# Optimization experiments

Measured on AMD Instinct MI355X. Metric: run time of the kernel, lower is better.

Reference implementation:

```python
import jax, jax.numpy as jnp
import numpy as np

HIDDEN_DIM = 128
NEIGHBOR_K = 2
N_ROWS = 1_000_000
BATCH = 262_144


def setup_inputs() -> dict:
    key = jax.random.key(0)
    k1, k2, k3, k4 = jax.random.split(key, 4)
    D = HIDDEN_DIM
    cat = D * (2 * NEIGHBOR_K + 1)  # 640
    x_rows = jax.random.normal(k1, (N_ROWS, D), dtype=jnp.float32)
    seed_indices = jax.random.randint(k2, (BATCH,), 0, N_ROWS)
    # torch.nn.Linear params: W [out, in], b [out]
    W1 = jax.random.normal(k3, (D, cat), dtype=jnp.float32) * (1.0 / np.sqrt(cat))
    b1 = jnp.zeros((D,), dtype=jnp.float32)
    W2 = jax.random.normal(k4, (D, D), dtype=jnp.float32) * (1.0 / np.sqrt(D))
    b2 = jnp.zeros((D,), dtype=jnp.float32)
    return {"x_rows": x_rows, "seed_indices": seed_indices,
            "W1": W1, "b1": b1, "W2": W2, "b2": b2}


def reference(x_rows, seed_indices, W1, b1, W2, b2):
    N, D = x_rows.shape
    B = seed_indices.shape[0]
    offsets = jnp.arange(-NEIGHBOR_K, NEIGHBOR_K + 1)  # [2k+1]
    idx = jnp.clip(seed_indices[:, None] + offsets[None, :], 0, N - 1)  # [B, 2k+1]
    # gather neighbor rows and flatten -> same as torch.cat(chunks, dim=-1)
    x_cat = x_rows[idx].reshape(B, (2 * NEIGHBOR_K + 1) * D)  # [B, 5D]
    h = jax.nn.relu(x_cat @ W1.T + b1)  # [B, D]
    return h @ W2.T + b2  # [B, D]
```

## Files before the change

kernel.cpp:

```cpp
#include <hip/hip_runtime.h>
#include <hip/hip_bf16.h>

#define D 128
#define CAT 640
#define BM 32
#define KS1 20
#define KS2 4
#define W1F_ELEMS 81920
#define W2F_ELEMS 16384

typedef __attribute__((ext_vector_type(8))) short bf16x8;
typedef __attribute__((ext_vector_type(4))) short short4v;
typedef __attribute__((ext_vector_type(4))) float f32x4;

static __device__ __forceinline__ unsigned short f32_to_bf16(float f) {
    unsigned u = __float_as_uint(f);
    unsigned r = u + 0x7FFFu + ((u >> 16) & 1u);
    return (unsigned short)(r >> 16);
}

__global__ void prep_frags(const float* __restrict__ W1, const float* __restrict__ W2,
                           unsigned short* __restrict__ W1f, unsigned short* __restrict__ W2f) {
    int f = blockIdx.x * 256 + threadIdx.x;
    if (f < W1F_ELEMS) {
        int e = f & 7, l = (f >> 3) & 63, j16 = (f >> 9) & 7, ks = f >> 12;
        int o = j16 * 16 + (l & 15);
        int k = ks * 32 + ((l >> 4) << 3) + e;
        W1f[f] = f32_to_bf16(W1[o * CAT + k]);
    } else if (f < W1F_ELEMS + W2F_ELEMS) {
        int f2 = f - W1F_ELEMS;
        int e = f2 & 7, l = (f2 >> 3) & 63, j16 = (f2 >> 9) & 7, ks = f2 >> 12;
        int o = j16 * 16 + (l & 15);
        int k = ks * 32 + ((l >> 4) << 3) + e;
        W2f[f2] = f32_to_bf16(W2[o * D + k]);
    }
}

__global__ __launch_bounds__(256) void rowmlp_kernel(
    const float* __restrict__ x_rows, const int* __restrict__ seeds,
    const unsigned short* __restrict__ W1f, const float* __restrict__ b1,
    const unsigned short* __restrict__ W2f, const float* __restrict__ b2,
    float* __restrict__ out, int B, int Nrows)
{
    __shared__ __align__(16) unsigned short Abuf[BM * CAT];
    __shared__ __align__(16) unsigned short Hbuf[BM * D];
    __shared__ int sseed[BM];

    const int tid = threadIdx.x;
    const int blk = blockIdx.x;

    if (tid < BM) sseed[tid] = seeds[blk * BM + tid];
    __syncthreads();

    {
        const int lane32 = tid & 31;
        const int segbase = tid >> 5;
        #pragma unroll
        for (int it = 0; it < BM * 5 / 8; ++it) {
            int seg = it * 8 + segbase;
            int row = seg / 5;
            int j = seg - row * 5;
            int idx = sseed[row] + j - 2;
            idx = idx < 0 ? 0 : (idx >= Nrows ? Nrows - 1 : idx);
            float4 v = *((const float4*)(x_rows + (size_t)idx * D) + lane32);
            short4v p;
            p.x = (short)f32_to_bf16(v.x);
            p.y = (short)f32_to_bf16(v.y);
            p.z = (short)f32_to_bf16(v.z);
            p.w = (short)f32_to_bf16(v.w);
            int kshort = j * D + lane32 * 4;
            int off = row * CAT + (kshort ^ ((row & 7) << 3));
            *(short4v*)(&Abuf[off]) = p;
        }
    }
    __syncthreads();

    const int wave = tid >> 6;
    const int l    = tid & 63;
    const int l15  = l & 15;
    const int lhi  = l >> 4;

    f32x4 acc[2][2] = {};
    #pragma unroll
    for (int ks = 0; ks < KS1; ++ks) {
        bf16x8 a[2], b[2];
        #pragma unroll
        for (int m = 0; m < 2; ++m) {
            int row = m * 16 + l15;
            int kshort = ks * 32 + lhi * 8;
            a[m] = *(const bf16x8*)(&Abuf[row * CAT + (kshort ^ ((row & 7) << 3))]);
        }
        #pragma unroll
        for (int n = 0; n < 2; ++n) {
            int j16 = wave * 2 + n;
            b[n] = ((const bf16x8*)W1f)[(ks * 8 + j16) * 64 + l];
        }
        #pragma unroll
        for (int m = 0; m < 2; ++m)
            #pragma unroll
            for (int n = 0; n < 2; ++n)
                acc[m][n] = __builtin_amdgcn_mfma_f32_16x16x32_bf16(a[m], b[n], acc[m][n], 0, 0, 0);
    }

    #pragma unroll
    for (int n = 0; n < 2; ++n) {
        int col = wave * 32 + n * 16 + l15;
        float bias = b1[col];
        #pragma unroll
        for (int m = 0; m < 2; ++m) {
            #pragma unroll
            for (int r = 0; r < 4; ++r) {
                float v = acc[m][n][r] + bias;
                v = v > 0.f ? v : 0.f;
                int row = m * 16 + lhi * 4 + r;
                Hbuf[row * D + (col ^ ((row & 7) << 3))] = f32_to_bf16(v);
            }
        }
    }
    __syncthreads();

    f32x4 acc2[2][2] = {};
    #pragma unroll
    for (int ks = 0; ks < KS2; ++ks) {
        bf16x8 a[2], b[2];
        #pragma unroll
        for (int m = 0; m < 2; ++m) {
            int row = m * 16 + l15;
            int kshort = ks * 32 + lhi * 8;
            a[m] = *(const bf16x8*)(&Hbuf[row * D + (kshort ^ ((row & 7) << 3))]);
        }
        #pragma unroll
        for (int n = 0; n < 2; ++n) {
            int j16 = wave * 2 + n;
            b[n] = ((const bf16x8*)W2f)[(ks * 8 + j16) * 64 + l];
        }
        #pragma unroll
        for (int m = 0; m < 2; ++m)
            #pragma unroll
            for (int n = 0; n < 2; ++n)
                acc2[m][n] = __builtin_amdgcn_mfma_f32_16x16x32_bf16(a[m], b[n], acc2[m][n], 0, 0, 0);
    }

    #pragma unroll
    for (int n = 0; n < 2; ++n) {
        int col = wave * 32 + n * 16 + l15;
        float bias = b2[col];
        #pragma unroll
        for (int m = 0; m < 2; ++m) {
            #pragma unroll
            for (int r = 0; r < 4; ++r) {
                int row = m * 16 + lhi * 4 + r;
                out[(size_t)(blk * BM + row) * D + col] = acc2[m][n][r] + bias;
            }
        }
    }
}

extern "C" void kernel_launch(void* const* d_in, const int* in_sizes, int n_in,
                              void* d_out, int out_size, void* d_ws, size_t ws_size,
                              hipStream_t stream) {
    const float* x_rows = (const float*)d_in[0];
    const int*   seeds  = (const int*)d_in[1];
    const float* W1     = (const float*)d_in[2];
    const float* b1     = (const float*)d_in[3];
    const float* W2     = (const float*)d_in[4];
    const float* b2     = (const float*)d_in[5];
    float* out = (float*)d_out;

    int Nrows = in_sizes[0] / D;
    int B = in_sizes[1];

    unsigned short* W1f = (unsigned short*)d_ws;
    unsigned short* W2f = W1f + W1F_ELEMS;

    prep_frags<<<(W1F_ELEMS + W2F_ELEMS + 255) / 256, 256, 0, stream>>>(W1, W2, W1f, W2f);
    rowmlp_kernel<<<B / BM, 256, 0, stream>>>(x_rows, seeds, W1f, b1, W2f, b2, out, B, Nrows);
}
```

Measured before the change: 197.2 us.

## Load gathered rows straight into MFMA A fragments, one 16-row tile per wave

Removes the shared-memory staging buffer for the gathered input. Each wave now owns 16 batch rows and loads its MFMA A operands directly from global memory, converting to bf16 in registers, and computes all 128 output columns itself. This eliminates the LDS write/read round trip and one block barrier, and shrinks shared memory so more blocks can be resident. In exchange, each wave reads all of W1/W2 for every 16 rows, so weight-fragment traffic per row doubles. The direct global loads are 32-byte chunks per lane rather than fully coalesced 512-byte rows.

```diff
diff --git a/kernel.cpp b/kernel.cpp
--- a/kernel.cpp
+++ b/kernel.cpp
@@ -3,14 +3,12 @@
 
 #define D 128
 #define CAT 640
-#define BM 32
 #define KS1 20
 #define KS2 4
 #define W1F_ELEMS 81920
 #define W2F_ELEMS 16384
 
 typedef __attribute__((ext_vector_type(8))) short bf16x8;
-typedef __attribute__((ext_vector_type(4))) short short4v;
 typedef __attribute__((ext_vector_type(4))) float f32x4;
 
 static __device__ __forceinline__ unsigned short f32_to_bf16(float f) {
@@ -40,118 +38,84 @@
     const float* __restrict__ x_rows, const int* __restrict__ seeds,
     const unsigned short* __restrict__ W1f, const float* __restrict__ b1,
     const unsigned short* __restrict__ W2f, const float* __restrict__ b2,
-    float* __restrict__ out, int B, int Nrows)
+    float* __restrict__ out, int Nrows)
 {
-    __shared__ __align__(16) unsigned short Abuf[BM * CAT];
-    __shared__ __align__(16) unsigned short Hbuf[BM * D];
-    __shared__ int sseed[BM];
+    __shared__ __align__(16) unsigned short Hbuf[4][16 * D];
 
     const int tid = threadIdx.x;
     const int blk = blockIdx.x;
+    const int g   = tid >> 6;
+    const int l   = tid & 63;
+    const int l15 = l & 15;
+    const int lhi = l >> 4;
 
-    if (tid < BM) sseed[tid] = seeds[blk * BM + tid];
-    __syncthreads();
+    const int sd = seeds[blk * 64 + g * 16 + l15];
+    unsigned roff[5];
+    #pragma unroll
+    for (int j = 0; j < 5; ++j) {
+        int idx = sd + j - 2;
+        idx = idx < 0 ? 0 : (idx >= Nrows ? Nrows - 1 : idx);
+        roff[j] = (unsigned)idx * (D * 4);
+    }
+    const char* xb = (const char*)x_rows;
+    const bf16x8* W1v = (const bf16x8*)W1f;
+    const bf16x8* W2v = (const bf16x8*)W2f;
 
-    {
-        const int lane32 = tid & 31;
-        const int segbase = tid >> 5;
+    f32x4 acc[8] = {};
+    #pragma unroll
+    for (int ks = 0; ks < KS1; ++ks) {
+        const int j = ks >> 2;
+        const float4* p = (const float4*)(xb + roff[j] + (ks & 3) * 128 + lhi * 32);
+        float4 p0 = p[0];
+        float4 p1 = p[1];
+        bf16x8 a;
+        a[0] = (short)f32_to_bf16(p0.x); a[1] = (short)f32_to_bf16(p0.y);
+        a[2] = (short)f32_to_bf16(p0.z); a[3] = (short)f32_to_bf16(p0.w);
+        a[4] = (short)f32_to_bf16(p1.x); a[5] = (short)f32_to_bf16(p1.y);
+        a[6] = (short)f32_to_bf16(p1.z); a[7] = (short)f32_to_bf16(p1.w);
         #pragma unroll
-        for (int it = 0; it < BM * 5 / 8; ++it) {
-            int seg = it * 8 + segbase;
-            int row = seg / 5;
-            int j = seg - row * 5;
-            int idx = sseed[row] + j - 2;
-            idx = idx < 0 ? 0 : (idx >= Nrows ? Nrows - 1 : idx);
-            float4 v = *((const float4*)(x_rows + (size_t)idx * D) + lane32);
-            short4v p;
-            p.x = (short)f32_to_bf16(v.x);
-            p.y = (short)f32_to_bf16(v.y);
-            p.z = (short)f32_to_bf16(v.z);
-            p.w = (short)f32_to_bf16(v.w);
-            int kshort = j * D + lane32 * 4;
-            int off = row * CAT + (kshort ^ ((row & 7) << 3));
-            *(short4v*)(&Abuf[off]) = p;
+        for (int n = 0; n < 8; ++n) {
+            bf16x8 b = W1v[(ks * 8 + n) * 64 + l];
+            acc[n] = __builtin_amdgcn_mfma_f32_16x16x32_bf16(a, b, acc[n], 0, 0, 0);
+        }
+    }
+
+    unsigned short* H = Hbuf[g];
+    #pragma unroll
+    for (int n = 0; n < 8; ++n) {
+        const int col = n * 16 + l15;
+        const float bias = b1[col];
+        #pragma unroll
+        for (int r = 0; r < 4; ++r) {
+            const int row = lhi * 4 + r;
+            float v = acc[n][r] + bias;
+            v = v > 0.f ? v : 0.f;
+            H[row * D + (col ^ ((row & 7) << 3))] = f32_to_bf16(v);
         }
     }
     __syncthreads();
 
-    const int wave = tid >> 6;
-    const int l    = tid & 63;
-    const int l15  = l & 15;
-    const int lhi  = l >> 4;
-
-    f32x4 acc[2][2] = {};
+    f32x4 acc2[8] = {};
     #pragma unroll
-    for (int ks = 0; ks < KS1; ++ks) {
-        bf16x8 a[2], b[2];
+    for (int ks = 0; ks < KS2; ++ks) {
+        const int row = l15;
+        bf16x8 a = *(const bf16x8*)(&H[row * D + ((ks * 32 + lhi * 8) ^ ((row & 7) << 3))]);
         #pragma unroll
-        for (int m = 0; m < 2; ++m) {
-            int row = m * 16 + l15;
-            int kshort = ks * 32 + lhi * 8;
-            a[m] = *(const bf16x8*)(&Abuf[row * CAT + (kshort ^ ((row & 7) << 3))]);
+        for (int n = 0; n < 8; ++n) {
+            bf16x8 b = W2v[(ks * 8 + n) * 64 + l];
+            acc2[n] = __builtin_amdgcn_mfma_f32_16x16x32_bf16(a, b, acc2[n], 0, 0, 0);
         }
-        #pragma unroll
-        for (int n = 0; n < 2; ++n) {
-            int j16 = wave * 2 + n;
-            b[n] = ((const bf16x8*)W1f)[(ks * 8 + j16) * 64 + l];
-        }
-        #pragma unroll
-        for (int m = 0; m < 2; ++m)
-            #pragma unroll
-            for (int n = 0; n < 2; ++n)
-                acc[m][n] = __builtin_amdgcn_mfma_f32_16x16x32_bf16(a[m], b[n], acc[m][n], 0, 0, 0);
     }
 
+    const size_t rowbase = (size_t)(blk * 64 + g * 16);
     #pragma unroll
-    for (int n = 0; n < 2; ++n) {
-        int col = wave * 32 + n * 16 + l15;
-        float bias = b1[col];
+    for (int n = 0; n < 8; ++n) {
+        const int col = n * 16 + l15;
+        const float bias = b2[col];
         #pragma unroll
-        for (int m = 0; m < 2; ++m) {
-            #pragma unroll
-            for (int r = 0; r < 4; ++r) {
-                float v = acc[m][n][r] + bias;
-                v = v > 0.f ? v : 0.f;
-                int row = m * 16 + lhi * 4 + r;
-                Hbuf[row * D + (col ^ ((row & 7) << 3))] = f32_to_bf16(v);
-            }
-        }
-    }
-    __syncthreads();
-
-    f32x4 acc2[2][2] = {};
-    #pragma unroll
-    for (int ks = 0; ks < KS2; ++ks) {
-        bf16x8 a[2], b[2];
-        #pragma unroll
-        for (int m = 0; m < 2; ++m) {
-            int row = m * 16 + l15;
-            int kshort = ks * 32 + lhi * 8;
-            a[m] = *(const bf16x8*)(&Hbuf[row * D + (kshort ^ ((row & 7) << 3))]);
-        }
-        #pragma unroll
-        for (int n = 0; n < 2; ++n) {
-            int j16 = wave * 2 + n;
-            b[n] = ((const bf16x8*)W2f)[(ks * 8 + j16) * 64 + l];
-        }
-        #pragma unroll
-        for (int m = 0; m < 2; ++m)
-            #pragma unroll
-            for (int n = 0; n < 2; ++n)
-                acc2[m][n] = __builtin_amdgcn_mfma_f32_16x16x32_bf16(a[m], b[n], acc2[m][n], 0, 0, 0);
-    }
-
-    #pragma unroll
-    for (int n = 0; n < 2; ++n) {
-        int col = wave * 32 + n * 16 + l15;
-        float bias = b2[col];
-        #pragma unroll
-        for (int m = 0; m < 2; ++m) {
-            #pragma unroll
-            for (int r = 0; r < 4; ++r) {
-                int row = m * 16 + lhi * 4 + r;
-                out[(size_t)(blk * BM + row) * D + col] = acc2[m][n][r] + bias;
-            }
+        for (int r = 0; r < 4; ++r) {
+            const int row = lhi * 4 + r;
+            out[(rowbase + row) * D + col] = acc2[n][r] + bias;
         }
     }
 }
@@ -174,5 +138,5 @@
     unsigned short* W2f = W1f + W1F_ELEMS;
 
     prep_frags<<<(W1F_ELEMS + W2F_ELEMS + 255) / 256, 256, 0, stream>>>(W1, W2, W1f, W2f);
-    rowmlp_kernel<<<B / BM, 256, 0, stream>>>(x_rows, seeds, W1f, b1, W2f, b2, out, B, Nrows);
+    rowmlp_kernel<<<B / 64, 256, 0, stream>>>(x_rows, seeds, W1f, b1, W2f, b2, out, Nrows);
 }
```

Result: slower. 250.4 us (+27.0%).

## Bucket-sort seeds by row range and remap workgroups per XCD for gather locality

Applied to the files above, without the earlier changes.

Seeds are bucketed into 4096 row-range buckets (256 rows each) through a histogram, scan and atomic scatter, so each workgroup gathers neighbouring rows of x_rows that are close together in memory. Workgroup ids are also remapped so that contiguous sorted blocks land on the same XCD, which is meant to improve L2 reuse of the overlapping neighbour rows. Outputs are written back to their original positions through the stored indices. This adds four small kernel launches, atomics and a scattered output write pattern.

```diff
diff --git a/kernel.cpp b/kernel.cpp
--- a/kernel.cpp
+++ b/kernel.cpp
@@ -4,10 +4,9 @@
 #define D 128
 #define CAT 640
 #define BM 32
-#define KS1 20
-#define KS2 4
 #define W1F_ELEMS 81920
 #define W2F_ELEMS 16384
+#define NBUCK 4096
 
 typedef __attribute__((ext_vector_type(8))) short bf16x8;
 typedef __attribute__((ext_vector_type(4))) short short4v;
@@ -36,27 +35,80 @@
     }
 }
 
+__global__ void zero_counts(int* __restrict__ counts) {
+    counts[blockIdx.x * 256 + threadIdx.x] = 0;
+}
+
+__global__ void hist_kernel(const int* __restrict__ seeds, int* __restrict__ counts, int B) {
+    int i = blockIdx.x * 256 + threadIdx.x;
+    if (i < B) atomicAdd(&counts[seeds[i] >> 8], 1);
+}
+
+__global__ __launch_bounds__(1024) void scan_kernel(const int* __restrict__ counts,
+                                                    int* __restrict__ offsets) {
+    __shared__ int tsum[1024];
+    const int tid = threadIdx.x;
+    int c0 = counts[tid * 4 + 0], c1 = counts[tid * 4 + 1];
+    int c2 = counts[tid * 4 + 2], c3 = counts[tid * 4 + 3];
+    int s = c0 + c1 + c2 + c3;
+    tsum[tid] = s;
+    __syncthreads();
+    for (int off = 1; off < 1024; off <<= 1) {
+        int v = 0;
+        if (tid >= off) v = tsum[tid - off];
+        __syncthreads();
+        if (tid >= off) tsum[tid] += v;
+        __syncthreads();
+    }
+    int excl = tsum[tid] - s;
+    offsets[tid * 4 + 0] = excl;
+    offsets[tid * 4 + 1] = excl + c0;
+    offsets[tid * 4 + 2] = excl + c0 + c1;
+    offsets[tid * 4 + 3] = excl + c0 + c1 + c2;
+}
+
+__global__ void scatter_kernel(const int* __restrict__ seeds, int* __restrict__ offsets,
+                               int2* __restrict__ sorted, int B) {
+    int i = blockIdx.x * 256 + threadIdx.x;
+    if (i < B) {
+        int s = seeds[i];
+        int pos = atomicAdd(&offsets[s >> 8], 1);
+        sorted[pos] = make_int2(s, i);
+    }
+}
+
 __global__ __launch_bounds__(256) void rowmlp_kernel(
-    const float* __restrict__ x_rows, const int* __restrict__ seeds,
+    const float* __restrict__ x_rows, const int2* __restrict__ sorted,
     const unsigned short* __restrict__ W1f, const float* __restrict__ b1,
     const unsigned short* __restrict__ W2f, const float* __restrict__ b2,
-    float* __restrict__ out, int B, int Nrows)
+    float* __restrict__ out, int Nrows, int nwg)
 {
-    __shared__ __align__(16) unsigned short Abuf[BM * CAT];
-    __shared__ __align__(16) unsigned short Hbuf[BM * D];
+    __shared__ __align__(16) unsigned short Ab[BM][CAT];
+    __shared__ __align__(16) unsigned short Hb[BM][D];
     __shared__ int sseed[BM];
+    __shared__ int sorig[BM];
 
     const int tid = threadIdx.x;
-    const int blk = blockIdx.x;
-
-    if (tid < BM) sseed[tid] = seeds[blk * BM + tid];
+    int blk;
+    {
+        int b = blockIdx.x;
+        int q = nwg >> 3, r = nwg & 7;
+        int xcd = b & 7, k = b >> 3;
+        blk = (xcd < r ? xcd * (q + 1) : r * (q + 1) + (xcd - r) * q) + k;
+    }
+
+    if (tid < BM) {
+        int2 sp = sorted[blk * BM + tid];
+        sseed[tid] = sp.x;
+        sorig[tid] = sp.y;
+    }
     __syncthreads();
 
     {
         const int lane32 = tid & 31;
         const int segbase = tid >> 5;
         #pragma unroll
-        for (int it = 0; it < BM * 5 / 8; ++it) {
+        for (int it = 0; it < 20; ++it) {
             int seg = it * 8 + segbase;
             int row = seg / 5;
             int j = seg - row * 5;
@@ -64,13 +116,10 @@
             idx = idx < 0 ? 0 : (idx >= Nrows ? Nrows - 1 : idx);
             float4 v = *((const float4*)(x_rows + (size_t)idx * D) + lane32);
             short4v p;
-            p.x = (short)f32_to_bf16(v.x);
-            p.y = (short)f32_to_bf16(v.y);
-            p.z = (short)f32_to_bf16(v.z);
-            p.w = (short)f32_to_bf16(v.w);
+            p[0] = (short)f32_to_bf16(v.x); p[1] = (short)f32_to_bf16(v.y);
+            p[2] = (short)f32_to_bf16(v.z); p[3] = (short)f32_to_bf16(v.w);
             int kshort = j * D + lane32 * 4;
-            int off = row * CAT + (kshort ^ ((row & 7) << 3));
-            *(short4v*)(&Abuf[off]) = p;
+            *(short4v*)(&Ab[row][kshort ^ ((row & 7) << 3)]) = p;
         }
     }
     __syncthreads();
@@ -80,20 +129,22 @@
     const int l15  = l & 15;
     const int lhi  = l >> 4;
 
+    const bf16x8* W1v = (const bf16x8*)W1f;
+    const bf16x8* W2v = (const bf16x8*)W2f;
+
     f32x4 acc[2][2] = {};
     #pragma unroll
-    for (int ks = 0; ks < KS1; ++ks) {
+    for (int ks = 0; ks < 20; ++ks) {
         bf16x8 a[2], b[2];
         #pragma unroll
         for (int m = 0; m < 2; ++m) {
             int row = m * 16 + l15;
-            int kshort = ks * 32 + lhi * 8;
-            a[m] = *(const bf16x8*)(&Abuf[row * CAT + (kshort ^ ((row & 7) << 3))]);
+            a[m] = *(const bf16x8*)(&Ab[row][(ks * 32 + lhi * 8) ^ ((row & 7) << 3)]);
         }
         #pragma unroll
         for (int n = 0; n < 2; ++n) {
             int j16 = wave * 2 + n;
-            b[n] = ((const bf16x8*)W1f)[(ks * 8 + j16) * 64 + l];
+            b[n] = W1v[(ks * 8 + j16) * 64 + l];
         }
         #pragma unroll
         for (int m = 0; m < 2; ++m)
@@ -113,7 +164,7 @@
                 float v = acc[m][n][r] + bias;
                 v = v > 0.f ? v : 0.f;
                 int row = m * 16 + lhi * 4 + r;
-                Hbuf[row * D + (col ^ ((row & 7) << 3))] = f32_to_bf16(v);
+                Hb[row][col ^ ((row & 7) << 3)] = f32_to_bf16(v);
             }
         }
     }
@@ -121,18 +172,17 @@
 
     f32x4 acc2[2][2] = {};
     #pragma unroll
-    for (int ks = 0; ks < KS2; ++ks) {
+    for (int ks = 0; ks < 4; ++ks) {
         bf16x8 a[2], b[2];
         #pragma unroll
         for (int m = 0; m < 2; ++m) {
             int row = m * 16 + l15;
-            int kshort = ks * 32 + lhi * 8;
-            a[m] = *(const bf16x8*)(&Hbuf[row * D + (kshort ^ ((row & 7) << 3))]);
+            a[m] = *(const bf16x8*)(&Hb[row][(ks * 32 + lhi * 8) ^ ((row & 7) << 3)]);
         }
         #pragma unroll
         for (int n = 0; n < 2; ++n) {
             int j16 = wave * 2 + n;
-            b[n] = ((const bf16x8*)W2f)[(ks * 8 + j16) * 64 + l];
+            b[n] = W2v[(ks * 8 + j16) * 64 + l];
         }
         #pragma unroll
         for (int m = 0; m < 2; ++m)
@@ -150,7 +200,7 @@
             #pragma unroll
             for (int r = 0; r < 4; ++r) {
                 int row = m * 16 + lhi * 4 + r;
-                out[(size_t)(blk * BM + row) * D + col] = acc2[m][n][r] + bias;
+                out[(size_t)sorig[row] * D + col] = acc2[m][n][r] + bias;
             }
         }
     }
@@ -172,7 +222,16 @@
 
     unsigned short* W1f = (unsigned short*)d_ws;
     unsigned short* W2f = W1f + W1F_ELEMS;
+    int* counts  = (int*)(W2f + W2F_ELEMS);
+    int* offsets = counts + NBUCK;
+    int2* sorted = (int2*)(offsets + NBUCK);
 
     prep_frags<<<(W1F_ELEMS + W2F_ELEMS + 255) / 256, 256, 0, stream>>>(W1, W2, W1f, W2f);
-    rowmlp_kernel<<<B / BM, 256, 0, stream>>>(x_rows, seeds, W1f, b1, W2f, b2, out, B, Nrows);
-}
+    zero_counts<<<NBUCK / 256, 256, 0, stream>>>(counts);
+    hist_kernel<<<(B + 255) / 256, 256, 0, stream>>>(seeds, counts, B);
+    scan_kernel<<<1, 1024, 0, stream>>>(counts, offsets);
+    scatter_kernel<<<(B + 255) / 256, 256, 0, stream>>>(seeds, offsets, sorted, B);
+
+    int nwg = B / BM;
+    rowmlp_kernel<<<nwg, 256, 0, stream>>>(x_rows, sorted, W1f, b1, W2f, b2, out, Nrows, nwg);
+}
```

New measurement: 230.6 us. 1.17x slower.

## Process four row tiles per block with register-staged gather prefetch overlapping MFMA

Applied to the files above, without the earlier changes.

Each block now handles four 32-row tiles instead of one. The gather of the next tile's neighbour rows is issued into two banks of register staging buffers while the current tile's two GEMMs run, then converted to bf16 and committed to shared memory between phases. This is meant to hide global gather latency behind MFMA work and to spread the per-block setup cost over more rows. In exchange it holds 80 extra VGPRs of staging data, sets a launch-bounds occupancy hint of 3, and shrinks the grid by a factor of four, which risks tail imbalance.

```diff
diff --git a/kernel.cpp b/kernel.cpp
--- a/kernel.cpp
+++ b/kernel.cpp
@@ -4,8 +4,7 @@
 #define D 128
 #define CAT 640
 #define BM 32
-#define KS1 20
-#define KS2 4
+#define G 4
 #define W1F_ELEMS 81920
 #define W2F_ELEMS 16384
 
@@ -36,124 +35,153 @@
     }
 }
 
-__global__ __launch_bounds__(256) void rowmlp_kernel(
+__global__ __launch_bounds__(256, 3) void rowmlp_kernel(
     const float* __restrict__ x_rows, const int* __restrict__ seeds,
     const unsigned short* __restrict__ W1f, const float* __restrict__ b1,
     const unsigned short* __restrict__ W2f, const float* __restrict__ b2,
-    float* __restrict__ out, int B, int Nrows)
+    float* __restrict__ out, int Nrows)
 {
-    __shared__ __align__(16) unsigned short Abuf[BM * CAT];
-    __shared__ __align__(16) unsigned short Hbuf[BM * D];
-    __shared__ int sseed[BM];
+    __shared__ __align__(16) unsigned short Ab[BM][CAT];
+    __shared__ __align__(16) unsigned short Hb[BM][D];
+    __shared__ int sseed[G * BM];
 
     const int tid = threadIdx.x;
     const int blk = blockIdx.x;
-
-    if (tid < BM) sseed[tid] = seeds[blk * BM + tid];
+    const int lane32  = tid & 31;
+    const int segbase = tid >> 5;
+
+    if (tid < G * BM) sseed[tid] = seeds[blk * (G * BM) + tid];
     __syncthreads();
 
-    {
-        const int lane32 = tid & 31;
-        const int segbase = tid >> 5;
-        #pragma unroll
-        for (int it = 0; it < BM * 5 / 8; ++it) {
-            int seg = it * 8 + segbase;
-            int row = seg / 5;
-            int j = seg - row * 5;
-            int idx = sseed[row] + j - 2;
-            idx = idx < 0 ? 0 : (idx >= Nrows ? Nrows - 1 : idx);
-            float4 v = *((const float4*)(x_rows + (size_t)idx * D) + lane32);
-            short4v p;
-            p.x = (short)f32_to_bf16(v.x);
-            p.y = (short)f32_to_bf16(v.y);
-            p.z = (short)f32_to_bf16(v.z);
-            p.w = (short)f32_to_bf16(v.w);
-            int kshort = j * D + lane32 * 4;
-            int off = row * CAT + (kshort ^ ((row & 7) << 3));
-            *(short4v*)(&Abuf[off]) = p;
-        }
-    }
-    __syncthreads();
+#define ISSUE(ST, g, IT0)                                                      \
+    _Pragma("unroll")                                                          \
+    for (int it = 0; it < 10; ++it) {                                          \
+        int seg = (it + IT0) * 8 + segbase;                                    \
+        int row = seg / 5;                                                     \
+        int j = seg - row * 5;                                                 \
+        int idx = sseed[(g) * BM + row] + j - 2;                               \
+        idx = idx < 0 ? 0 : (idx >= Nrows ? Nrows - 1 : idx);                  \
+        ST[it] = *((const float4*)(x_rows + (size_t)idx * D) + lane32);        \
+    }
+
+#define COMMIT(ST, IT0)                                                        \
+    _Pragma("unroll")                                                          \
+    for (int it = 0; it < 10; ++it) {                                          \
+        int seg = (it + IT0) * 8 + segbase;                                    \
+        int row = seg / 5;                                                     \
+        int j = seg - row * 5;                                                 \
+        short4v p;                                                             \
+        p[0] = (short)f32_to_bf16(ST[it].x); p[1] = (short)f32_to_bf16(ST[it].y); \
+        p[2] = (short)f32_to_bf16(ST[it].z); p[3] = (short)f32_to_bf16(ST[it].w); \
+        int kshort = j * D + lane32 * 4;                                       \
+        *(short4v*)(&Ab[row][kshort ^ ((row & 7) << 3)]) = p;                  \
+    }
 
     const int wave = tid >> 6;
     const int l    = tid & 63;
     const int l15  = l & 15;
     const int lhi  = l >> 4;
 
-    f32x4 acc[2][2] = {};
-    #pragma unroll
-    for (int ks = 0; ks < KS1; ++ks) {
-        bf16x8 a[2], b[2];
-        #pragma unroll
-        for (int m = 0; m < 2; ++m) {
-            int row = m * 16 + l15;
-            int kshort = ks * 32 + lhi * 8;
-            a[m] = *(const bf16x8*)(&Abuf[row * CAT + (kshort ^ ((row & 7) << 3))]);
-        }
+    const bf16x8* W1v = (const bf16x8*)W1f;
+    const bf16x8* W2v = (const bf16x8*)W2f;
+
+    float4 st_a[10], st_b[10];
+
+    ISSUE(st_a, 0, 0)
+    ISSUE(st_b, 0, 10)
+    COMMIT(st_a, 0)
+    COMMIT(st_b, 10)
+    __syncthreads();
+
+    for (int g = 0; g < G; ++g) {
+        if (g < G - 1) ISSUE(st_a, g + 1, 0)
+
+        f32x4 acc[2][2] = {};
+        #pragma unroll
+        for (int ks = 0; ks < 20; ++ks) {
+            bf16x8 a[2], b[2];
+            #pragma unroll
+            for (int m = 0; m < 2; ++m) {
+                int row = m * 16 + l15;
+                a[m] = *(const bf16x8*)(&Ab[row][(ks * 32 + lhi * 8) ^ ((row & 7) << 3)]);
+            }
+            #pragma unroll
+            for (int n = 0; n < 2; ++n) {
+                int j16 = wave * 2 + n;
+                b[n] = W1v[(ks * 8 + j16) * 64 + l];
+            }
+            #pragma unroll
+            for (int m = 0; m < 2; ++m)
+                #pragma unroll
+                for (int n = 0; n < 2; ++n)
+                    acc[m][n] = __builtin_amdgcn_mfma_f32_16x16x32_bf16(a[m], b[n], acc[m][n], 0, 0, 0);
+        }
+
         #pragma unroll
         for (int n = 0; n < 2; ++n) {
-            int j16 = wave * 2 + n;
-            b[n] = ((const bf16x8*)W1f)[(ks * 8 + j16) * 64 + l];
-        }
-        #pragma unroll
-        for (int m = 0; m < 2; ++m)
-            #pragma unroll
-            for (int n = 0; n < 2; ++n)
-                acc[m][n] = __builtin_amdgcn_mfma_f32_16x16x32_bf16(a[m], b[n], acc[m][n], 0, 0, 0);
-    }
-
-    #pragma unroll
-    for (int n = 0; n < 2; ++n) {
-        int col = wave * 32 + n * 16 + l15;
-        float bias = b1[col];
-        #pragma unroll
-        for (int m = 0; m < 2; ++m) {
-            #pragma unroll
-            for (int r = 0; r < 4; ++r) {
-                float v = acc[m][n][r] + bias;
-                v = v > 0.f ? v : 0.f;
-                int row = m * 16 + lhi * 4 + r;
-                Hbuf[row * D + (col ^ ((row & 7) << 3))] = f32_to_bf16(v);
-            }
-        }
-    }
-    __syncthreads();
-
-    f32x4 acc2[2][2] = {};
-    #pragma unroll
-    for (int ks = 0; ks < KS2; ++ks) {
-        bf16x8 a[2], b[2];
-        #pragma unroll
-        for (int m = 0; m < 2; ++m) {
-            int row = m * 16 + l15;
-            int kshort = ks * 32 + lhi * 8;
-            a[m] = *(const bf16x8*)(&Hbuf[row * D + (kshort ^ ((row & 7) << 3))]);
-        }
+            int col = wave * 32 + n * 16 + l15;
+            float bias = b1[col];
+            #pragma unroll
+            for (int m = 0; m < 2; ++m) {
+                #pragma unroll
+                for (int r = 0; r < 4; ++r) {
+                    float v = acc[m][n][r] + bias;
+                    v = v > 0.f ? v : 0.f;
+                    int row = m * 16 + lhi * 4 + r;
+                    Hb[row][col ^ ((row & 7) << 3)] = f32_to_bf16(v);
+                }
+            }
+        }
+        __syncthreads();
+
+        if (g < G - 1) {
+            COMMIT(st_a, 0)
+            ISSUE(st_b, g + 1, 10)
+        }
+
+        f32x4 acc2[2][2] = {};
+        #pragma unroll
+        for (int ks = 0; ks < 4; ++ks) {
+            bf16x8 a[2], b[2];
+            #pragma unroll
+            for (int m = 0; m < 2; ++m) {
+                int row = m * 16 + l15;
+                a[m] = *(const bf16x8*)(&Hb[row][(ks * 32 + lhi * 8) ^ ((row & 7) << 3)]);
+            }
+            #pragma unroll
+            for (int n = 0; n < 2; ++n) {
+                int j16 = wave * 2 + n;
+                b[n] = W2v[(ks * 8 + j16) * 64 + l];
+            }
+            #pragma unroll
+            for (int m = 0; m < 2; ++m)
+                #pragma unroll
+                for (int n = 0; n < 2; ++n)
+                    acc2[m][n] = __builtin_amdgcn_mfma_f32_16x16x32_bf16(a[m], b[n], acc2[m][n], 0, 0, 0);
+        }
+
+        const size_t rowbase = (size_t)blk * (G * BM) + g * BM;
         #pragma unroll
         for (int n = 0; n < 2; ++n) {
-            int j16 = wave * 2 + n;
-            b[n] = ((const bf16x8*)W2f)[(ks * 8 + j16) * 64 + l];
-        }
-        #pragma unroll
-        for (int m = 0; m < 2; ++m)
-            #pragma unroll
-            for (int n = 0; n < 2; ++n)
-                acc2[m][n] = __builtin_amdgcn_mfma_f32_16x16x32_bf16(a[m], b[n], acc2[m][n], 0, 0, 0);
-    }
-
-    #pragma unroll
-    for (int n = 0; n < 2; ++n) {
-        int col = wave * 32 + n * 16 + l15;
-        float bias = b2[col];
-        #pragma unroll
-        for (int m = 0; m < 2; ++m) {
-            #pragma unroll
-            for (int r = 0; r < 4; ++r) {
-                int row = m * 16 + lhi * 4 + r;
-                out[(size_t)(blk * BM + row) * D + col] = acc2[m][n][r] + bias;
-            }
-        }
-    }
+            int col = wave * 32 + n * 16 + l15;
+            float bias = b2[col];
+            #pragma unroll
+            for (int m = 0; m < 2; ++m) {
+                #pragma unroll
+                for (int r = 0; r < 4; ++r) {
+                    int row = m * 16 + lhi * 4 + r;
+                    out[(rowbase + row) * D + col] = acc2[m][n][r] + bias;
+                }
+            }
+        }
+
+        if (g < G - 1) {
+            COMMIT(st_b, 10)
+            __syncthreads();
+        }
+    }
+#undef ISSUE
+#undef COMMIT
 }
 
 extern "C" void kernel_launch(void* const* d_in, const int* in_sizes, int n_in,
@@ -174,5 +202,5 @@
     unsigned short* W2f = W1f + W1F_ELEMS;
 
     prep_frags<<<(W1F_ELEMS + W2F_ELEMS + 255) / 256, 256, 0, stream>>>(W1, W2, W1f, W2f);
-    rowmlp_kernel<<<B / BM, 256, 0, stream>>>(x_rows, seeds, W1f, b1, W2f, b2, out, B, Nrows);
-}
+    rowmlp_kernel<<<B / (G * BM), 256, 0, stream>>>(x_rows, seeds, W1f, b1, W2f, b2, out, Nrows);
+}
```

After: 586.7 us. 2.98x slower.
